# Kernel tuning notes

Hardware: AMD Instinct MI355X
Metric: run time of the kernel (lower is better)

## Reference

```python
import jax, jax.numpy as jnp
import numpy as np

SCALE = 0.125  # 1/sqrt(d_head=64)

def setup_inputs() -> dict:
    key = jax.random.key(0)
    kq, kk, kv = jax.random.split(key, 3)
    B, S, D = 16, 2048, 64
    q = jax.random.normal(kq, (B, S, D), dtype=jnp.float32)
    k = jax.random.normal(kk, (B, S, D), dtype=jnp.float32)
    v = jax.random.normal(kv, (B, S, D), dtype=jnp.float32)
    return {"q": q, "k": k, "v": v}

def reference(q, k, v):
    # scores: [B, S, S] = q @ k^T * scale
    scores = jnp.einsum('bqd,bkd->bqk', q, k) * SCALE
    attention = jax.nn.softmax(scores, axis=2)
    # dropout p=0.0 -> identity (eval); attn_mask=None -> no masking
    context = jnp.einsum('bqk,bkd->bqd', attention, v)
    return (context, attention)
```

## Files before the change

kernel.cpp:

```cpp
#include <hip/hip_runtime.h>

#define BB 16
#define SS 2048
#define DD 64
#define L2E 1.44269504f
#define A3C 4.32808512f

typedef _Float16 half8 __attribute__((ext_vector_type(8)));
typedef _Float16 half4 __attribute__((ext_vector_type(4)));
typedef float f32x4 __attribute__((ext_vector_type(4)));

typedef const __attribute__((address_space(1))) void* gas_ptr;
typedef __attribute__((address_space(3))) void* las_ptr;

#define TILE_SYNC(N)                                            \
  do {                                                          \
    asm volatile("s_waitcnt vmcnt(" #N ")" ::: "memory");       \
    __builtin_amdgcn_s_barrier();                               \
    __builtin_amdgcn_sched_barrier(0);                          \
  } while (0)

__global__ __launch_bounds__(256) void setup_kernel(const float* __restrict__ K,
                                                    const float* __restrict__ V,
                                                    _Float16* __restrict__ Kh,
                                                    _Float16* __restrict__ VT) {
  __shared__ float tile[64][65];
  int b = blockIdx.x >> 5, kt = blockIdx.x & 31;
  int tid = threadIdx.x;
  size_t base = ((size_t)b * SS + (size_t)kt * 64) * DD;
  const float4* Kq = (const float4*)(K + base);
  const float4* Vq = (const float4*)(V + base);
  half4* Khq = (half4*)(Kh + base);
#pragma unroll
  for (int it = 0; it < 4; ++it) {
    int i = tid + it * 256;
    float4 kv = Kq[i];
    half4 h;
    h[0] = (_Float16)kv.x; h[1] = (_Float16)kv.y;
    h[2] = (_Float16)kv.z; h[3] = (_Float16)kv.w;
    Khq[i] = h;
    float4 vv = Vq[i];
    int row = i >> 4, c4 = (i & 15) << 2;
    tile[row][c4 + 0] = vv.x; tile[row][c4 + 1] = vv.y;
    tile[row][c4 + 2] = vv.z; tile[row][c4 + 3] = vv.w;
  }
  __syncthreads();
  int d = tid >> 2, seg = tid & 3;
  half8 o0, o1;
#pragma unroll
  for (int j = 0; j < 8; ++j) o0[j] = (_Float16)tile[seg * 16 + j][d];
#pragma unroll
  for (int j = 0; j < 8; ++j) o1[j] = (_Float16)tile[seg * 16 + 8 + j][d];
  _Float16* dst = VT + ((size_t)b * DD + d) * SS + (size_t)kt * 64 + seg * 16;
  *(half8*)dst = o0;
  *(half8*)(dst + 8) = o1;
}

__device__ __forceinline__ void stage64(const _Float16* __restrict__ gbase, size_t rstride,
                                        _Float16* lds, int tid) {
  int w = tid >> 6, lam = tid & 63;
#pragma unroll
  for (int a = 0; a < 2; ++a) {
    int rloc = lam >> 3;
    int r = w * 16 + a * 8 + rloc;
    int byt = ((lam & 7) * 16) ^ (rloc << 4);
    const _Float16* g = gbase + (size_t)r * rstride + (byt >> 1);
    _Float16* lp = lds + (w * 16 + a * 8) * 64;
    __builtin_amdgcn_global_load_lds((gas_ptr)g, (las_ptr)lp, 16, 0, 0);
  }
}

__device__ __forceinline__ void load_qfrag(const float* __restrict__ Qp,
                                           half8& qa0, half8& qa1) {
  float4 v0 = *(const float4*)(Qp);
  float4 v1 = *(const float4*)(Qp + 4);
  float4 v2 = *(const float4*)(Qp + 32);
  float4 v3 = *(const float4*)(Qp + 36);
  qa0[0] = (_Float16)(v0.x * 0.125f); qa0[1] = (_Float16)(v0.y * 0.125f);
  qa0[2] = (_Float16)(v0.z * 0.125f); qa0[3] = (_Float16)(v0.w * 0.125f);
  qa0[4] = (_Float16)(v1.x * 0.125f); qa0[5] = (_Float16)(v1.y * 0.125f);
  qa0[6] = (_Float16)(v1.z * 0.125f); qa0[7] = (_Float16)(v1.w * 0.125f);
  qa1[0] = (_Float16)(v2.x * 0.125f); qa1[1] = (_Float16)(v2.y * 0.125f);
  qa1[2] = (_Float16)(v2.z * 0.125f); qa1[3] = (_Float16)(v2.w * 0.125f);
  qa1[4] = (_Float16)(v3.x * 0.125f); qa1[5] = (_Float16)(v3.y * 0.125f);
  qa1[6] = (_Float16)(v3.z * 0.125f); qa1[7] = (_Float16)(v3.w * 0.125f);
}

__global__ __launch_bounds__(256, 2) void attn_kernel(const float* __restrict__ Q,
                                                      const _Float16* __restrict__ Kh,
                                                      const _Float16* __restrict__ VT,
                                                      float* __restrict__ ctx_out,
                                                      float* __restrict__ attn_out) {
  __shared__ __attribute__((aligned(16))) _Float16 Kl[4][64 * 64];
  __shared__ __attribute__((aligned(16))) _Float16 Vl[3][64 * 64];

  int tid = threadIdx.x;
  int w = tid >> 6, l = tid & 63, g = l >> 4, c = l & 15;
  int bid = (int)blockIdx.x;
  int remap = (bid & 7) * 64 + (bid >> 3);
  int b = remap >> 5, qb = remap & 31;
  size_t qr = (size_t)b * SS + (size_t)qb * 64 + (size_t)w * 16;
  const _Float16* KB = Kh + (size_t)b * SS * DD;
  const _Float16* VB = VT + (size_t)b * DD * SS;
  int swz = (c & 7) << 4;

  stage64(KB, DD, Kl[0], tid);
  stage64(KB + (size_t)64 * DD, DD, Kl[1], tid);
  stage64(KB + (size_t)128 * DD, DD, Kl[2], tid);

  half8 qa0, qa1;
  load_qfrag(Q + (qr + c) * DD + 8 * g, qa0, qa1);

  float lsum = 0.f;
  for (int t = 0; t < 32; ++t) {
    if (t < 30) TILE_SYNC(4);
    else if (t == 30) TILE_SYNC(2);
    else TILE_SYNC(0);
    if (t + 3 < 32) stage64(KB + (size_t)(t + 3) * 64 * DD, DD, Kl[(t + 3) & 3], tid);
    const _Float16* kl = Kl[t & 3];
    __builtin_amdgcn_s_setprio(1);
#pragma unroll
    for (int kt = 0; kt < 4; ++kt) {
      const _Float16* kb = kl + (kt * 16 + c) * 64;
      half8 kf0 = *(const half8*)(kb + (((16 * g) ^ swz) >> 1));
      half8 kf1 = *(const half8*)(kb + (((64 + 16 * g) ^ swz) >> 1));
      f32x4 s = {0.f, 0.f, 0.f, 0.f};
      s = __builtin_amdgcn_mfma_f32_16x16x32_f16(kf0, qa0, s, 0, 0, 0);
      s = __builtin_amdgcn_mfma_f32_16x16x32_f16(kf1, qa1, s, 0, 0, 0);
      lsum += exp2f(fmaf(s[0], L2E, -A3C)) + exp2f(fmaf(s[1], L2E, -A3C)) +
              exp2f(fmaf(s[2], L2E, -A3C)) + exp2f(fmaf(s[3], L2E, -A3C));
    }
    __builtin_amdgcn_s_setprio(0);
  }
  lsum += __shfl_xor(lsum, 16);
  lsum += __shfl_xor(lsum, 32);
  float ac = -__log2f(lsum) - A3C;

  stage64(VB, SS, Vl[0], tid);
  stage64(VB + 64, SS, Vl[1], tid);

  __syncthreads();

  stage64(KB, DD, Kl[0], tid);
  stage64(KB + (size_t)64 * DD, DD, Kl[1], tid);

  f32x4 cacc[4] = {{0.f, 0.f, 0.f, 0.f}, {0.f, 0.f, 0.f, 0.f},
                   {0.f, 0.f, 0.f, 0.f}, {0.f, 0.f, 0.f, 0.f}};
  int bufc = 0, bufs = 2;
  for (int t = 0; t < 32; ++t) {
    if (t == 0) TILE_SYNC(2);
    else if (t == 1) TILE_SYNC(8);
    else if (t < 31) TILE_SYNC(12);
    else TILE_SYNC(4);
    if (t + 2 < 32) {
      stage64(KB + (size_t)(t + 2) * 64 * DD, DD, Kl[bufs], tid);
      stage64(VB + (size_t)(t + 2) * 64, SS, Vl[bufs], tid);
    }
    const _Float16* kl = Kl[bufc];
    const _Float16* vl = Vl[bufc];
    __builtin_amdgcn_s_setprio(1);
#pragma unroll
    for (int kt = 0; kt < 4; ++kt) {
      const _Float16* kb = kl + (kt * 16 + c) * 64;
      half8 kf0 = *(const half8*)(kb + (((16 * g) ^ swz) >> 1));
      half8 kf1 = *(const half8*)(kb + (((64 + 16 * g) ^ swz) >> 1));
      f32x4 s = {0.f, 0.f, 0.f, 0.f};
      s = __builtin_amdgcn_mfma_f32_16x16x32_f16(kf0, qa0, s, 0, 0, 0);
      s = __builtin_amdgcn_mfma_f32_16x16x32_f16(kf1, qa1, s, 0, 0, 0);

      float p0 = exp2f(fmaf(s[0], L2E, ac));
      float p1 = exp2f(fmaf(s[1], L2E, ac));
      float p2 = exp2f(fmaf(s[2], L2E, ac));
      float p3 = exp2f(fmaf(s[3], L2E, ac));
      f32x4 st = {p0, p1, p2, p3};
      *(f32x4*)(attn_out + (qr + c) * SS + t * 64 + kt * 16 + 4 * g) = st;

      half4 pf;
      pf[0] = (_Float16)p0; pf[1] = (_Float16)p1;
      pf[2] = (_Float16)p2; pf[3] = (_Float16)p3;
#pragma unroll
      for (int dt = 0; dt < 4; ++dt) {
        const _Float16* vb = vl + (dt * 16 + c) * 64;
        half4 vf = *(const half4*)(vb + (((32 * kt + 8 * g) ^ swz) >> 1));
        cacc[dt] = __builtin_amdgcn_mfma_f32_16x16x16f16(pf, vf, cacc[dt], 0, 0, 0);
      }
    }
    __builtin_amdgcn_s_setprio(0);
    bufc = (bufc == 2) ? 0 : bufc + 1;
    bufs = (bufs == 2) ? 0 : bufs + 1;
  }

#pragma unroll
  for (int dt = 0; dt < 4; ++dt)
#pragma unroll
    for (int j = 0; j < 4; ++j)
      ctx_out[(qr + 4 * g + j) * DD + dt * 16 + c] = cacc[dt][j];
}

extern "C" void kernel_launch(void* const* d_in, const int* in_sizes, int n_in,
                              void* d_out, int out_size, void* d_ws, size_t ws_size,
                              hipStream_t stream) {
  const float* q = (const float*)d_in[0];
  const float* k = (const float*)d_in[1];
  const float* v = (const float*)d_in[2];
  float* ctx = (float*)d_out;
  float* attn = ctx + (size_t)BB * SS * DD;
  _Float16* Kh = (_Float16*)d_ws;
  _Float16* VT = Kh + (size_t)BB * SS * DD;
  setup_kernel<<<dim3(BB * 32), dim3(256), 0, stream>>>(k, v, Kh, VT);
  attn_kernel<<<dim3(BB * 32), dim3(256), 0, stream>>>(q, Kh, VT, ctx, attn);
}
```

Before: 101.3 us.

## Halve attention block to 32 query rows with shallower shared-memory pipeline

Each attention block now handles 32 query rows with 128 threads instead of 64 rows with 256 threads, so the grid doubles. Each stage64 call now loads a full 64-row K or V tile using 4 loads per thread. Shared memory drops to four 8 KB slabs: three-deep K staging in the first pass and double-buffered K/V in the second. The aim is higher occupancy and more blocks to hide latency. The cost is twice the K/V reloads from L2 per query row, a shallower prefetch, and s_setprio removed.

Measured after the change: 94.93 us, median of 2. 6.3% less time.

```diff
diff --git a/kernel.cpp b/kernel.cpp
--- a/kernel.cpp
+++ b/kernel.cpp
@@ -12,6 +12,8 @@
 
 typedef const __attribute__((address_space(1))) void* gas_ptr;
 typedef __attribute__((address_space(3))) void* las_ptr;
+
+#define SBAR() __builtin_amdgcn_sched_barrier(0)
 
 #define TILE_SYNC(N)                                            \
   do {                                                          \
@@ -60,12 +62,12 @@
                                         _Float16* lds, int tid) {
   int w = tid >> 6, lam = tid & 63;
 #pragma unroll
-  for (int a = 0; a < 2; ++a) {
+  for (int a = 0; a < 4; ++a) {
     int rloc = lam >> 3;
-    int r = w * 16 + a * 8 + rloc;
+    int r = w * 32 + a * 8 + rloc;
     int byt = ((lam & 7) * 16) ^ (rloc << 4);
     const _Float16* g = gbase + (size_t)r * rstride + (byt >> 1);
-    _Float16* lp = lds + (w * 16 + a * 8) * 64;
+    _Float16* lp = lds + (w * 32 + a * 8) * 64;
     __builtin_amdgcn_global_load_lds((gas_ptr)g, (las_ptr)lp, 16, 0, 0);
   }
 }
@@ -86,39 +88,39 @@
   qa1[6] = (_Float16)(v3.z * 0.125f); qa1[7] = (_Float16)(v3.w * 0.125f);
 }
 
-__global__ __launch_bounds__(256, 2) void attn_kernel(const float* __restrict__ Q,
+__global__ __launch_bounds__(128, 2) void attn_kernel(const float* __restrict__ Q,
                                                       const _Float16* __restrict__ Kh,
                                                       const _Float16* __restrict__ VT,
                                                       float* __restrict__ ctx_out,
                                                       float* __restrict__ attn_out) {
-  __shared__ __attribute__((aligned(16))) _Float16 Kl[4][64 * 64];
-  __shared__ __attribute__((aligned(16))) _Float16 Vl[3][64 * 64];
+  __shared__ __attribute__((aligned(16))) _Float16 slab[4][64 * 64];
 
   int tid = threadIdx.x;
   int w = tid >> 6, l = tid & 63, g = l >> 4, c = l & 15;
   int bid = (int)blockIdx.x;
-  int remap = (bid & 7) * 64 + (bid >> 3);
-  int b = remap >> 5, qb = remap & 31;
-  size_t qr = (size_t)b * SS + (size_t)qb * 64 + (size_t)w * 16;
+  int remap = (bid & 7) * 128 + (bid >> 3);
+  int b = remap >> 6, qb = remap & 63;
+  size_t qr = (size_t)b * SS + (size_t)qb * 32 + (size_t)w * 16;
   const _Float16* KB = Kh + (size_t)b * SS * DD;
   const _Float16* VB = VT + (size_t)b * DD * SS;
   int swz = (c & 7) << 4;
 
-  stage64(KB, DD, Kl[0], tid);
-  stage64(KB + (size_t)64 * DD, DD, Kl[1], tid);
-  stage64(KB + (size_t)128 * DD, DD, Kl[2], tid);
-
   half8 qa0, qa1;
   load_qfrag(Q + (qr + c) * DD + 8 * g, qa0, qa1);
+  SBAR();
+  stage64(KB, DD, slab[0], tid);
+  SBAR();
+  stage64(KB + (size_t)64 * DD, DD, slab[1], tid);
+  SBAR();
 
   float lsum = 0.f;
   for (int t = 0; t < 32; ++t) {
-    if (t < 30) TILE_SYNC(4);
-    else if (t == 30) TILE_SYNC(2);
-    else TILE_SYNC(0);
-    if (t + 3 < 32) stage64(KB + (size_t)(t + 3) * 64 * DD, DD, Kl[(t + 3) & 3], tid);
-    const _Float16* kl = Kl[t & 3];
-    __builtin_amdgcn_s_setprio(1);
+    if (t < 31) TILE_SYNC(4); else TILE_SYNC(0);
+    if (t + 2 < 32) {
+      stage64(KB + (size_t)(t + 2) * 64 * DD, DD, slab[(t + 2) & 3], tid);
+      SBAR();
+    }
+    const _Float16* kl = slab[t & 3];
 #pragma unroll
     for (int kt = 0; kt < 4; ++kt) {
       const _Float16* kb = kl + (kt * 16 + c) * 64;
@@ -130,35 +132,31 @@
       lsum += exp2f(fmaf(s[0], L2E, -A3C)) + exp2f(fmaf(s[1], L2E, -A3C)) +
               exp2f(fmaf(s[2], L2E, -A3C)) + exp2f(fmaf(s[3], L2E, -A3C));
     }
-    __builtin_amdgcn_s_setprio(0);
   }
   lsum += __shfl_xor(lsum, 16);
   lsum += __shfl_xor(lsum, 32);
   float ac = -__log2f(lsum) - A3C;
 
-  stage64(VB, SS, Vl[0], tid);
-  stage64(VB + 64, SS, Vl[1], tid);
-
   __syncthreads();
 
-  stage64(KB, DD, Kl[0], tid);
-  stage64(KB + (size_t)64 * DD, DD, Kl[1], tid);
+  stage64(KB, DD, slab[0], tid);
+  stage64(VB, SS, slab[2], tid);
+  SBAR();
+  stage64(KB + (size_t)64 * DD, DD, slab[1], tid);
+  stage64(VB + 64, SS, slab[3], tid);
+  SBAR();
 
   f32x4 cacc[4] = {{0.f, 0.f, 0.f, 0.f}, {0.f, 0.f, 0.f, 0.f},
                    {0.f, 0.f, 0.f, 0.f}, {0.f, 0.f, 0.f, 0.f}};
-  int bufc = 0, bufs = 2;
   for (int t = 0; t < 32; ++t) {
-    if (t == 0) TILE_SYNC(2);
-    else if (t == 1) TILE_SYNC(8);
-    else if (t < 31) TILE_SYNC(12);
-    else TILE_SYNC(4);
-    if (t + 2 < 32) {
-      stage64(KB + (size_t)(t + 2) * 64 * DD, DD, Kl[bufs], tid);
-      stage64(VB + (size_t)(t + 2) * 64, SS, Vl[bufs], tid);
-    }
-    const _Float16* kl = Kl[bufc];
-    const _Float16* vl = Vl[bufc];
-    __builtin_amdgcn_s_setprio(1);
+    if (t == 0) TILE_SYNC(8); else TILE_SYNC(4);
+    if (t >= 1 && t <= 30) {
+      stage64(KB + (size_t)(t + 1) * 64 * DD, DD, slab[(t + 1) & 1], tid);
+      stage64(VB + (size_t)(t + 1) * 64, SS, slab[2 + ((t + 1) & 1)], tid);
+      SBAR();
+    }
+    const _Float16* kl = slab[t & 1];
+    const _Float16* vl = slab[2 + (t & 1)];
 #pragma unroll
     for (int kt = 0; kt < 4; ++kt) {
       const _Float16* kb = kl + (kt * 16 + c) * 64;
@@ -185,9 +183,6 @@
         cacc[dt] = __builtin_amdgcn_mfma_f32_16x16x16f16(pf, vf, cacc[dt], 0, 0, 0);
       }
     }
-    __builtin_amdgcn_s_setprio(0);
-    bufc = (bufc == 2) ? 0 : bufc + 1;
-    bufs = (bufs == 2) ? 0 : bufs + 1;
   }
 
 #pragma unroll
@@ -208,5 +203,5 @@
   _Float16* Kh = (_Float16*)d_ws;
   _Float16* VT = Kh + (size_t)BB * SS * DD;
   setup_kernel<<<dim3(BB * 32), dim3(256), 0, stream>>>(k, v, Kh, VT);
-  attn_kernel<<<dim3(BB * 32), dim3(256), 0, stream>>>(q, Kh, VT, ctx, attn);
-}
+  attn_kernel<<<dim3(BB * 64), dim3(128), 0, stream>>>(q, Kh, VT, ctx, attn);
+}
```
